# Kernel optimization log

Hardware: AMD Instinct MI355X
Metric: run time of the kernel (lower is better)

## Reference

```python
import math
import jax, jax.numpy as jnp
import numpy as np

HEADS = 8
DIM = 512
HEAD_SIZE = DIM // HEADS  # 64


def setup_inputs() -> dict:
    key = jax.random.key(0)
    ks = jax.random.split(key, 5)
    b, nh, nw, t, d = 16, 16, 16, 16, DIM
    x = jax.random.normal(ks[0], (b, nh, nw, t, d), dtype=jnp.float32)
    s = 1.0 / math.sqrt(d)
    Wq = jax.random.normal(ks[1], (d, d), dtype=jnp.float32) * s
    Wk = jax.random.normal(ks[2], (d, d), dtype=jnp.float32) * s
    Wv = jax.random.normal(ks[3], (d, d), dtype=jnp.float32) * s
    Wo = jax.random.normal(ks[4], (d, d), dtype=jnp.float32) * s
    z = jnp.zeros((d,), dtype=jnp.float32)
    return {"x": x, "Wq": Wq, "bq": z, "Wk": Wk, "bk": z, "Wv": Wv, "bv": z, "Wo": Wo, "bo": z}


def _split_heads(t):
    # [b, n1, n2, T, D] -> [b, n1, n2, H, T, hs]
    b, n1, n2, T, _ = t.shape
    return t.reshape(b, n1, n2, T, HEADS, HEAD_SIZE).transpose(0, 1, 2, 4, 3, 5)


def reference(x, Wq, bq, Wk, bk, Wv, bv, Wo, bo):
    q = _split_heads(x @ Wq + bq)
    k = _split_heads(x @ Wk + bk)
    v = _split_heads(x @ Wv + bv)
    # windowed attention scores: [b, n1, n2, H, T, T]
    scores = jnp.einsum('bnmhtd,bnmhsd->bnmhts', q, k) / math.sqrt(HEAD_SIZE)
    probs = jax.nn.sigmoid(scores)  # NOTE: elementwise sigmoid, not softmax
    ctx = jnp.einsum('bnmhts,bnmhsd->bnmhtd', probs, v)
    b, n1, n2, H, T, hs = ctx.shape
    ctx = ctx.transpose(0, 1, 2, 4, 3, 5).reshape(b, n1, n2, T, H * hs)
    return ctx @ Wo + bo
```

## Files before the change

### kernel.cpp

```cpp
#include <hip/hip_runtime.h>
#include <hip/hip_bf16.h>

typedef float f32x4 __attribute__((ext_vector_type(4)));
typedef __bf16 bf16x8 __attribute__((ext_vector_type(8)));
typedef unsigned short u16x4 __attribute__((ext_vector_type(4)));
typedef unsigned short u16x8 __attribute__((ext_vector_type(8)));

__device__ __forceinline__ unsigned short f2bf(float f) {
  union { float f; unsigned u; } x; x.f = f;
  unsigned r = x.u + 0x7FFFu + ((x.u >> 16) & 1u);
  return (unsigned short)(r >> 16);
}

__device__ __forceinline__ void gl16(const void* g, void* l) {
  __builtin_amdgcn_global_load_lds(
      (const __attribute__((address_space(1))) unsigned*)g,
      (__attribute__((address_space(3))) unsigned*)l, 16, 0, 0);
}

__global__ __launch_bounds__(256) void prep_wt(const float* __restrict__ Wq,
                                               const float* __restrict__ Wk,
                                               const float* __restrict__ Wv,
                                               const float* __restrict__ Wo,
                                               unsigned short* __restrict__ WT) {
  __shared__ unsigned short ts[64][65];
  const float* W = (blockIdx.z == 0) ? Wq : (blockIdx.z == 1) ? Wk
                   : (blockIdx.z == 2) ? Wv : Wo;
  const int t = threadIdx.x;
  const int kbase = blockIdx.y * 64;
  const int nbase = blockIdx.x * 64;
  for (int i = 0; i < 16; ++i) {
    int idx = i * 256 + t;
    int r = idx >> 6, c = idx & 63;
    ts[r][c] = f2bf(W[(size_t)(kbase + r) * 512 + nbase + c]);
  }
  __syncthreads();
  unsigned short* dst = WT + (size_t)blockIdx.z * 512 * 512;
  for (int i = 0; i < 16; ++i) {
    int idx = i * 256 + t;
    int nn = idx >> 6, kk = idx & 63;
    dst[(size_t)(nbase + nn) * 512 + kbase + kk] = ts[kk][nn];
  }
}

__global__ void prep_bias(const float* __restrict__ bq, const float* __restrict__ bk,
                          const float* __restrict__ bv, float* __restrict__ biasc) {
  int i = blockIdx.x * 256 + threadIdx.x;
  if (i < 512) biasc[i] = bq[i];
  else if (i < 1024) biasc[i] = bk[i - 512];
  else if (i < 1536) biasc[i] = bv[i - 1024];
}

__global__ __launch_bounds__(256) void convert_x(const float* __restrict__ x,
                                                 unsigned short* __restrict__ xb,
                                                 long long n8) {
  long long i = (long long)blockIdx.x * 256 + threadIdx.x;
  const long long stride = (long long)gridDim.x * 256;
  for (; i < n8; i += stride) {
    f32x4 a = *reinterpret_cast<const f32x4*>(&x[i * 8]);
    f32x4 b = *reinterpret_cast<const f32x4*>(&x[i * 8 + 4]);
    u16x8 o;
    o[0] = f2bf(a[0]); o[1] = f2bf(a[1]); o[2] = f2bf(a[2]); o[3] = f2bf(a[3]);
    o[4] = f2bf(b[0]); o[5] = f2bf(b[1]); o[6] = f2bf(b[2]); o[7] = f2bf(b[3]);
    *reinterpret_cast<u16x8*>(&xb[i * 8]) = o;
  }
}

template <typename CT>
__global__ __launch_bounds__(512, 2) void gemm256(
    const unsigned short* __restrict__ A, int lda,
    const unsigned short* __restrict__ BT,
    CT* __restrict__ C, int ldc,
    const float* __restrict__ bias, int NB) {
  __shared__ alignas(16) unsigned short pool[66048];
  const int t = threadIdx.x;
  const int lane = t & 63;
  const int w = t >> 6;
  const int wm = w >> 2, wn = w & 3;

  const int nwg = gridDim.x;
  const int cpx = nwg >> 3;
  const int wg = (blockIdx.x & 7) * cpx + (blockIdx.x >> 3);
  const int n0 = (wg % NB) * 256;
  const int m0 = (wg / NB) * 256;

  const int sr = lane >> 3;
  const int sg = ((lane & 7) ^ sr) << 3;
  const unsigned short* gA = A + (size_t)(m0 + w * 8 + sr) * lda + sg;
  const unsigned short* gB = BT + (size_t)(n0 + w * 8 + sr) * 512 + sg;
  const int lw = w * 512;

#define STAGE_A(kt, h, b)                                                   \
  { const unsigned short* g_ = gA + (size_t)(h) * 128 * lda + (kt) * 64;    \
    unsigned short* l_ = &pool[(b) * 16384 + (h) * 8192 + lw];              \
    gl16(g_, l_); gl16(g_ + (size_t)64 * lda, l_ + 4096); }
#define STAGE_B(kt, h, b)                                                   \
  { const unsigned short* g_ = gB + (size_t)(h) * 128 * 512 + (kt) * 64;    \
    unsigned short* l_ = &pool[32768 + (b) * 16384 + (h) * 8192 + lw];      \
    gl16(g_, l_); gl16(g_ + (size_t)64 * 512, l_ + 4096); }

  const int fr = lane & 15;
  const int fg = lane >> 4;
  const int fx = lane & 7;
  auto readA = [&](int b, int mi, int kf) -> bf16x8 {
    return *reinterpret_cast<const bf16x8*>(
        &pool[(b) * 16384 + (wm * 128 + mi * 16 + fr) * 64 +
              ((((kf << 2) + fg) ^ fx) << 3)]);
  };
  auto readB = [&](int b, int ni, int kf) -> bf16x8 {
    return *reinterpret_cast<const bf16x8*>(
        &pool[32768 + (b) * 16384 + (wn * 64 + ni * 16 + fr) * 64 +
              ((((kf << 2) + fg) ^ fx) << 3)]);
  };

  f32x4 acc[8][4];
#pragma unroll
  for (int i = 0; i < 8; ++i)
#pragma unroll
    for (int j = 0; j < 4; ++j) acc[i][j] = (f32x4){0.f, 0.f, 0.f, 0.f};
  bf16x8 bfr[4][2];

#define PHASE(b, q, READB, STAGES, VM)                                       \
  {                                                                          \
    bf16x8 a0_ = readA(b, 2 * (q), 0), a1_ = readA(b, 2 * (q), 1);           \
    bf16x8 a2_ = readA(b, 2 * (q) + 1, 0), a3_ = readA(b, 2 * (q) + 1, 1);   \
    if (READB) {                                                             \
      _Pragma("unroll") for (int ni = 0; ni < 4; ++ni) {                     \
        bfr[ni][0] = readB(b, ni, 0);                                        \
        bfr[ni][1] = readB(b, ni, 1);                                        \
      }                                                                      \
    }                                                                        \
    STAGES;                                                                  \
    if ((VM) == 4) asm volatile("s_waitcnt vmcnt(4)" ::: "memory");          \
    if ((VM) == 0) asm volatile("s_waitcnt vmcnt(0)" ::: "memory");          \
    __builtin_amdgcn_s_barrier();                                            \
    asm volatile("s_waitcnt lgkmcnt(0)" ::: "memory");                       \
    __builtin_amdgcn_sched_barrier(0);                                       \
    __builtin_amdgcn_s_setprio(1);                                           \
    _Pragma("unroll") for (int ni = 0; ni < 4; ++ni) {                       \
      acc[2 * (q)][ni] = __builtin_amdgcn_mfma_f32_16x16x32_bf16(            \
          a0_, bfr[ni][0], acc[2 * (q)][ni], 0, 0, 0);                       \
      acc[2 * (q) + 1][ni] = __builtin_amdgcn_mfma_f32_16x16x32_bf16(        \
          a2_, bfr[ni][0], acc[2 * (q) + 1][ni], 0, 0, 0);                   \
    }                                                                        \
    _Pragma("unroll") for (int ni = 0; ni < 4; ++ni) {                       \
      acc[2 * (q)][ni] = __builtin_amdgcn_mfma_f32_16x16x32_bf16(            \
          a1_, bfr[ni][1], acc[2 * (q)][ni], 0, 0, 0);                       \
      acc[2 * (q) + 1][ni] = __builtin_amdgcn_mfma_f32_16x16x32_bf16(        \
          a3_, bfr[ni][1], acc[2 * (q) + 1][ni], 0, 0, 0);                   \
    }                                                                        \
    __builtin_amdgcn_s_setprio(0);                                           \
    __builtin_amdgcn_s_barrier();                                            \
  }

  STAGE_B(0, 0, 0); STAGE_B(0, 1, 0);
  STAGE_A(0, 0, 0); STAGE_A(0, 1, 0);
  STAGE_B(1, 0, 1); STAGE_B(1, 1, 1);
  asm volatile("s_waitcnt vmcnt(4)" ::: "memory");
  __builtin_amdgcn_s_barrier();

#pragma unroll
  for (int i = 0; i < 4; ++i) {
    const bool s2 = (i < 3);
    const int vmA = s2 ? 4 : 0;
    const int vmB = s2 ? 4 : 0;
    PHASE(0, 0, true,  { STAGE_A(2 * i + 1, 0, 1) }, -1);
    PHASE(0, 1, false, { STAGE_A(2 * i + 1, 1, 1) if (s2) STAGE_B(2 * i + 2, 0, 0) }, -1);
    PHASE(0, 2, false, { if (s2) STAGE_B(2 * i + 2, 1, 0) }, -1);
    PHASE(0, 3, false, {}, vmA);
    PHASE(1, 0, true,  { if (s2) STAGE_A(2 * i + 2, 0, 0) }, -1);
    PHASE(1, 1, false, { if (s2) STAGE_A(2 * i + 2, 1, 0) }, -1);
    PHASE(1, 2, false, { if (s2) STAGE_B(2 * i + 3, 0, 1) }, -1);
    PHASE(1, 3, false, { if (s2) STAGE_B(2 * i + 3, 1, 1) }, vmB);
  }
#undef PHASE
#undef STAGE_A
#undef STAGE_B

  __syncthreads();
  if constexpr (sizeof(CT) == 2) {
#pragma unroll
    for (int ni = 0; ni < 4; ++ni) {
      int cl = wn * 64 + ni * 16 + fr;
      float bc = bias[n0 + cl];
#pragma unroll
      for (int mi = 0; mi < 8; ++mi) {
        int rl = wm * 128 + mi * 16 + fg * 4;
#pragma unroll
        for (int r = 0; r < 4; ++r)
          pool[(rl + r) * 258 + cl] = f2bf(acc[mi][ni][r] + bc);
      }
    }
    __syncthreads();
#pragma unroll
    for (int it = 0; it < 16; ++it) {
      int idx = it * 512 + t;
      int row = idx >> 5, c8 = idx & 31;
      u16x8 v = *reinterpret_cast<const u16x8*>(&pool[row * 258 + c8 * 8]);
      *reinterpret_cast<u16x8*>(&C[(size_t)(m0 + row) * ldc + n0 + c8 * 8]) = v;
    }
  } else {
    float* stf = reinterpret_cast<float*>(pool);
#pragma unroll
    for (int h = 0; h < 2; ++h) {
      if (wm == h) {
#pragma unroll
        for (int ni = 0; ni < 4; ++ni) {
          int cl = wn * 64 + ni * 16 + fr;
          float bc = bias[n0 + cl];
#pragma unroll
          for (int mi = 0; mi < 8; ++mi) {
            int rl = mi * 16 + fg * 4;
#pragma unroll
            for (int r = 0; r < 4; ++r)
              stf[(rl + r) * 258 + cl] = acc[mi][ni][r] + bc;
          }
        }
      }
      __syncthreads();
#pragma unroll
      for (int it = 0; it < 16; ++it) {
        int idx = it * 512 + t;
        int row = idx >> 6, c4 = idx & 63;
        f32x4 v = *reinterpret_cast<const f32x4*>(&stf[row * 258 + c4 * 4]);
        *reinterpret_cast<f32x4*>(
            &C[(size_t)(m0 + h * 128 + row) * ldc + n0 + c4 * 4]) = v;
      }
      __syncthreads();
    }
  }
}

__global__ __launch_bounds__(256) void attn2(unsigned short* __restrict__ QKV) {
  __shared__ alignas(16) unsigned short sh[33792];
  const int VS = 16384, PS = 32768;
  const int t = threadIdx.x;
  const int lane = t & 63;
  const int w = t >> 6;
  const int fr = lane & 15, fg = lane >> 4, fx = lane & 7;
  const int sr = lane >> 3;
  const int sgx = ((lane & 7) ^ sr) << 3;
  const int sgl = (lane & 7) << 3;
  const size_t m0r = (size_t)blockIdx.x * 128;

#define SK2(h, b)                                                            \
  _Pragma("unroll") for (int u = 0; u < 4; ++u) {                            \
    const int r0 = u * 32 + w * 8;                                           \
    gl16(QKV + (m0r + r0 + sr) * 1536 + 512 + (h) * 64 + sgx,                \
         &sh[(b) * 8192 + r0 * 64]);                                         \
  }
#define SV2(h, b)                                                            \
  _Pragma("unroll") for (int u = 0; u < 4; ++u) {                            \
    const int r0 = u * 32 + w * 8;                                           \
    gl16(QKV + (m0r + r0 + sr) * 1536 + 1024 + (h) * 64 + sgl,               \
         &sh[VS + (b) * 8192 + r0 * 64]);                                    \
  }

  SK2(0, 0) SV2(0, 0)
  asm volatile("s_waitcnt vmcnt(0)" ::: "memory");
  __syncthreads();

  for (int h = 0; h < 8; ++h) {
    const int b = h & 1;
    u16x8 q[2][2];
#pragma unroll
    for (int ww = 0; ww < 2; ++ww) {
      const int wi = w * 2 + ww;
      const unsigned short* qrow = QKV + (m0r + wi * 16 + fr) * 1536 + h * 64;
      q[ww][0] = *reinterpret_cast<const u16x8*>(qrow + fg * 8);
      q[ww][1] = *reinterpret_cast<const u16x8*>(qrow + 32 + fg * 8);
    }
    if (h < 7) { SK2(h + 1, b ^ 1) SV2(h + 1, b ^ 1) }

#pragma unroll
    for (int ww = 0; ww < 2; ++ww) {
      const int wi = w * 2 + ww;
      f32x4 s = (f32x4){0.f, 0.f, 0.f, 0.f};
      {
        bf16x8 kf_ = *reinterpret_cast<const bf16x8*>(
            &sh[b * 8192 + (wi * 16 + fr) * 64 + ((fg ^ fx) << 3)]);
        s = __builtin_amdgcn_mfma_f32_16x16x32_bf16(
            kf_, __builtin_bit_cast(bf16x8, q[ww][0]), s, 0, 0, 0);
        kf_ = *reinterpret_cast<const bf16x8*>(
            &sh[b * 8192 + (wi * 16 + fr) * 64 + (((4 + fg) ^ fx) << 3)]);
        s = __builtin_amdgcn_mfma_f32_16x16x32_bf16(
            kf_, __builtin_bit_cast(bf16x8, q[ww][1]), s, 0, 0, 0);
      }
      u16x4 pfu;
#pragma unroll
      for (int r = 0; r < 4; ++r)
        pfu[r] = f2bf(1.0f / (1.0f + __expf(-s[r] * 0.125f)));
      *reinterpret_cast<u16x4*>(&sh[PS + w * 256 + fr * 16 + fg * 4]) = pfu;
      u16x8 pbu = (u16x8){0, 0, 0, 0, 0, 0, 0, 0};
      if (fg < 2)
        pbu = *reinterpret_cast<const u16x8*>(&sh[PS + w * 256 + fr * 16 + fg * 8]);
      bf16x8 pb = __builtin_bit_cast(bf16x8, pbu);
#pragma unroll
      for (int dc = 0; dc < 4; ++dc) {
        u16x8 vau;
#pragma unroll
        for (int j = 0; j < 8; ++j)
          vau[j] = sh[VS + b * 8192 + (wi * 16 + (fg & 1) * 8 + j) * 64 + dc * 16 + fr];
        f32x4 c = __builtin_amdgcn_mfma_f32_16x16x32_bf16(
            __builtin_bit_cast(bf16x8, vau), pb, (f32x4){0.f, 0.f, 0.f, 0.f},
            0, 0, 0);
        u16x4 o;
#pragma unroll
        for (int r = 0; r < 4; ++r) o[r] = f2bf(c[r]);
        *reinterpret_cast<u16x4*>(
            &QKV[(m0r + wi * 16 + fr) * 1536 + 1024 + h * 64 + dc * 16 + fg * 4]) = o;
      }
    }
    asm volatile("s_waitcnt vmcnt(8)" ::: "memory");
    __syncthreads();
  }
#undef SK2
#undef SV2
}

extern "C" void kernel_launch(void* const* d_in, const int* in_sizes, int n_in,
                              void* d_out, int out_size, void* d_ws, size_t ws_size,
                              hipStream_t stream) {
  const float* x  = (const float*)d_in[0];
  const float* Wq = (const float*)d_in[1];
  const float* bq = (const float*)d_in[2];
  const float* Wk = (const float*)d_in[3];
  const float* bk = (const float*)d_in[4];
  const float* Wv = (const float*)d_in[5];
  const float* bv = (const float*)d_in[6];
  const float* Wo = (const float*)d_in[7];
  const float* bo = (const float*)d_in[8];
  float* out = (float*)d_out;

  const int M = 65536;
  char* ws = (char*)d_ws;
  unsigned short* WT = (unsigned short*)ws;
  float* biasc = (float*)(ws + (size_t)2048 * 512 * 2);
  const long long prep_bytes = (long long)2048 * 512 * 2 + 8192;

  prep_wt<<<dim3(8, 8, 4), 256, 0, stream>>>(Wq, Wk, Wv, Wo, WT);
  prep_bias<<<6, 256, 0, stream>>>(bq, bk, bv, biasc);

  long long avail = (long long)ws_size - prep_bytes;
  int chunk_rows = 65536;
  while (chunk_rows > 2048 && (long long)chunk_rows * 4096 > avail) chunk_rows >>= 1;
  const int nchunks = M / chunk_rows;

  unsigned short* Xb  = (unsigned short*)(ws + prep_bytes);
  unsigned short* QKV = Xb + (size_t)chunk_rows * 512;

  for (int c = 0; c < nchunks; ++c) {
    const size_t row0 = (size_t)c * chunk_rows;
    const int mt = chunk_rows / 256;
    convert_x<<<2048, 256, 0, stream>>>(x + row0 * 512, Xb,
                                        (long long)chunk_rows * 64);
    gemm256<unsigned short><<<mt * 6, 512, 0, stream>>>(
        Xb, 512, WT, QKV, 1536, biasc, 6);
    attn2<<<chunk_rows / 128, 256, 0, stream>>>(QKV);
    gemm256<float><<<mt * 2, 512, 0, stream>>>(
        QKV + 1024, 1536, WT + (size_t)1536 * 512, out + row0 * 512, 512, bo, 2);
  }
}
```

Measured before the change: 293.8 us.

## Fuse fp32-to-bf16 conversion of x into the QKV projection GEMM

Removes the separate convert_x kernel and adds a QKV GEMM variant that loads fp32 activations straight into registers, converts them to bf16 and writes them into swizzled LDS, interleaved with the MFMA phases. This drops the bf16 copy of x (a write plus a re-read of 64 MB of bf16) and shrinks the workspace needed per chunk. In exchange the GEMM reads fp32 A, twice the bytes per tile, and each of the 6 N-tiles per row block re-reads it. The A path also uses register staging instead of direct global-to-LDS loads, which adds VGPR pressure and conversion ALU work inside the pipelined loop.

```diff
diff --git a/kernel.cpp b/kernel.cpp
--- a/kernel.cpp
+++ b/kernel.cpp
@@ -51,18 +51,154 @@
   else if (i < 1536) biasc[i] = bv[i - 1024];
 }
 
-__global__ __launch_bounds__(256) void convert_x(const float* __restrict__ x,
-                                                 unsigned short* __restrict__ xb,
-                                                 long long n8) {
-  long long i = (long long)blockIdx.x * 256 + threadIdx.x;
-  const long long stride = (long long)gridDim.x * 256;
-  for (; i < n8; i += stride) {
-    f32x4 a = *reinterpret_cast<const f32x4*>(&x[i * 8]);
-    f32x4 b = *reinterpret_cast<const f32x4*>(&x[i * 8 + 4]);
-    u16x8 o;
-    o[0] = f2bf(a[0]); o[1] = f2bf(a[1]); o[2] = f2bf(a[2]); o[3] = f2bf(a[3]);
-    o[4] = f2bf(b[0]); o[5] = f2bf(b[1]); o[6] = f2bf(b[2]); o[7] = f2bf(b[3]);
-    *reinterpret_cast<u16x8*>(&xb[i * 8]) = o;
+__global__ __launch_bounds__(512, 2) void gemm256_f32a(
+    const float* __restrict__ A, int lda,
+    const unsigned short* __restrict__ BT,
+    unsigned short* __restrict__ C, int ldc,
+    const float* __restrict__ bias, int NB) {
+  __shared__ alignas(16) unsigned short pool[66048];
+  const int t = threadIdx.x;
+  const int lane = t & 63;
+  const int w = t >> 6;
+  const int wm = w >> 2, wn = w & 3;
+
+  const int nwg = gridDim.x;
+  const int cpx = nwg >> 3;
+  const int wg = (blockIdx.x & 7) * cpx + (blockIdx.x >> 3);
+  const int n0 = (wg % NB) * 256;
+  const int m0 = (wg / NB) * 256;
+
+  const int sr = lane >> 3;
+  const int sg = ((lane & 7) ^ sr) << 3;
+  const unsigned short* gB = BT + (size_t)(n0 + w * 8 + sr) * 512 + sg;
+  const int lw = w * 512;
+#define SBa(kt, b)                                                          \
+  { const unsigned short* g_ = gB + (kt) * 64;                              \
+    unsigned short* l_ = &pool[32768 + (b) * 16384 + lw];                   \
+    gl16(g_, l_); gl16(g_ + (size_t)64 * 512, l_ + 4096); }
+#define SBb(kt, b)                                                          \
+  { const unsigned short* g_ = gB + (size_t)128 * 512 + (kt) * 64;          \
+    unsigned short* l_ = &pool[32768 + (b) * 16384 + 8192 + lw];            \
+    gl16(g_, l_); gl16(g_ + (size_t)64 * 512, l_ + 4096); }
+
+  const int arow = t >> 3;
+  const int aseg = t & 7;
+  const float* gA = A + (size_t)(m0 + arow) * lda + ((aseg ^ (arow & 7)) << 3);
+  f32x4 ar0[8], ar1[8];
+#define LA(u, arr, kt)                                                      \
+  { const float* g_ = gA + (size_t)(u) * 64 * lda + (kt) * 64;              \
+    arr[2 * (u)] = *reinterpret_cast<const f32x4*>(g_);                     \
+    arr[2 * (u) + 1] = *reinterpret_cast<const f32x4*>(g_ + 4); }
+#define WAu(u, arr, b)                                                      \
+  { bf16x8 pk_;                                                             \
+    _Pragma("unroll") for (int j_ = 0; j_ < 4; ++j_) {                      \
+      pk_[j_] = (__bf16)arr[2 * (u)][j_];                                   \
+      pk_[4 + j_] = (__bf16)arr[2 * (u) + 1][j_];                           \
+    }                                                                       \
+    *reinterpret_cast<bf16x8*>(                                             \
+        &pool[(b) * 16384 + (arow + (u) * 64) * 64 + (aseg << 3)]) = pk_; }
+
+  const int fr = lane & 15;
+  const int fg = lane >> 4;
+  const int fx = lane & 7;
+  auto readA = [&](int b, int mi, int kf) -> bf16x8 {
+    return *reinterpret_cast<const bf16x8*>(
+        &pool[(b) * 16384 + (wm * 128 + mi * 16 + fr) * 64 +
+              ((((kf << 2) + fg) ^ fx) << 3)]);
+  };
+  auto readB = [&](int b, int ni, int kf) -> bf16x8 {
+    return *reinterpret_cast<const bf16x8*>(
+        &pool[32768 + (b) * 16384 + (wn * 64 + ni * 16 + fr) * 64 +
+              ((((kf << 2) + fg) ^ fx) << 3)]);
+  };
+
+  f32x4 acc[8][4];
+#pragma unroll
+  for (int i = 0; i < 8; ++i)
+#pragma unroll
+    for (int j = 0; j < 4; ++j) acc[i][j] = (f32x4){0.f, 0.f, 0.f, 0.f};
+  bf16x8 bfr[4][2];
+
+#define PHASEF(b, q, READB, STAGES, VM)                                      \
+  {                                                                          \
+    bf16x8 a0_ = readA(b, 2 * (q), 0), a1_ = readA(b, 2 * (q), 1);           \
+    bf16x8 a2_ = readA(b, 2 * (q) + 1, 0), a3_ = readA(b, 2 * (q) + 1, 1);   \
+    if (READB) {                                                             \
+      _Pragma("unroll") for (int ni = 0; ni < 4; ++ni) {                     \
+        bfr[ni][0] = readB(b, ni, 0);                                        \
+        bfr[ni][1] = readB(b, ni, 1);                                        \
+      }                                                                      \
+    }                                                                        \
+    STAGES;                                                                  \
+    if ((VM) == 12)                                                          \
+      asm volatile("s_waitcnt vmcnt(12) lgkmcnt(0)" ::: "memory");           \
+    if ((VM) == 0)                                                           \
+      asm volatile("s_waitcnt vmcnt(0) lgkmcnt(0)" ::: "memory");            \
+    __builtin_amdgcn_s_barrier();                                            \
+    asm volatile("s_waitcnt lgkmcnt(0)" ::: "memory");                       \
+    __builtin_amdgcn_sched_barrier(0);                                       \
+    __builtin_amdgcn_s_setprio(1);                                           \
+    _Pragma("unroll") for (int ni = 0; ni < 4; ++ni) {                       \
+      acc[2 * (q)][ni] = __builtin_amdgcn_mfma_f32_16x16x32_bf16(            \
+          a0_, bfr[ni][0], acc[2 * (q)][ni], 0, 0, 0);                       \
+      acc[2 * (q) + 1][ni] = __builtin_amdgcn_mfma_f32_16x16x32_bf16(        \
+          a2_, bfr[ni][0], acc[2 * (q) + 1][ni], 0, 0, 0);                   \
+    }                                                                        \
+    _Pragma("unroll") for (int ni = 0; ni < 4; ++ni) {                       \
+      acc[2 * (q)][ni] = __builtin_amdgcn_mfma_f32_16x16x32_bf16(            \
+          a1_, bfr[ni][1], acc[2 * (q)][ni], 0, 0, 0);                       \
+      acc[2 * (q) + 1][ni] = __builtin_amdgcn_mfma_f32_16x16x32_bf16(        \
+          a3_, bfr[ni][1], acc[2 * (q) + 1][ni], 0, 0, 0);                   \
+    }                                                                        \
+    __builtin_amdgcn_s_setprio(0);                                           \
+    __builtin_amdgcn_s_barrier();                                            \
+  }
+
+  LA(0, ar0, 0) LA(1, ar0, 0) LA(2, ar0, 0) LA(3, ar0, 0)
+  LA(0, ar1, 1) LA(1, ar1, 1) LA(2, ar1, 1) LA(3, ar1, 1)
+  SBa(0, 0) SBb(0, 0) SBa(1, 1) SBb(1, 1)
+  WAu(0, ar0, 0) WAu(1, ar0, 0) WAu(2, ar0, 0) WAu(3, ar0, 0)
+  asm volatile("s_waitcnt vmcnt(4) lgkmcnt(0)" ::: "memory");
+  __builtin_amdgcn_s_barrier();
+
+#pragma unroll
+  for (int i = 0; i < 4; ++i) {
+    const bool s2 = (i < 3);
+    PHASEF(0, 0, true,  { if (s2) { LA(0, ar0, 2 * i + 2) LA(1, ar0, 2 * i + 2) } }, -1);
+    PHASEF(0, 1, false, { if (s2) { LA(2, ar0, 2 * i + 2) LA(3, ar0, 2 * i + 2) SBa(2 * i + 2, 0) } }, -1);
+    PHASEF(0, 2, false, { WAu(0, ar1, 1) WAu(1, ar1, 1) if (s2) SBb(2 * i + 2, 0) }, -1);
+    PHASEF(0, 3, false, { WAu(2, ar1, 1) WAu(3, ar1, 1) }, s2 ? 12 : 0);
+    PHASEF(1, 0, true,  { if (s2) { LA(0, ar1, 2 * i + 3) LA(1, ar1, 2 * i + 3) } }, -1);
+    PHASEF(1, 1, false, { if (s2) { LA(2, ar1, 2 * i + 3) LA(3, ar1, 2 * i + 3) } }, -1);
+    PHASEF(1, 2, false, { if (s2) { SBa(2 * i + 3, 1) WAu(0, ar0, 0) WAu(1, ar0, 0) } }, -1);
+    PHASEF(1, 3, false, { if (s2) { SBb(2 * i + 3, 1) WAu(2, ar0, 0) WAu(3, ar0, 0) } }, s2 ? 12 : -1);
+  }
+#undef PHASEF
+#undef SBa
+#undef SBb
+#undef LA
+#undef WAu
+
+  __syncthreads();
+#pragma unroll
+  for (int ni = 0; ni < 4; ++ni) {
+    int cl = wn * 64 + ni * 16 + fr;
+    float bc = bias[n0 + cl];
+#pragma unroll
+    for (int mi = 0; mi < 8; ++mi) {
+      int rl = wm * 128 + mi * 16 + fg * 4;
+#pragma unroll
+      for (int r = 0; r < 4; ++r)
+        pool[(rl + r) * 258 + cl] = f2bf(acc[mi][ni][r] + bc);
+    }
+  }
+  __syncthreads();
+#pragma unroll
+  for (int it = 0; it < 16; ++it) {
+    int idx = it * 512 + t;
+    int row = idx >> 5, c8 = idx & 31;
+    u16x8 v = *reinterpret_cast<const u16x8*>(&pool[row * 258 + c8 * 8]);
+    *reinterpret_cast<u16x8*>(&C[(size_t)(m0 + row) * ldc + n0 + c8 * 8]) = v;
   }
 }
 
@@ -343,19 +479,16 @@
 
   long long avail = (long long)ws_size - prep_bytes;
   int chunk_rows = 65536;
-  while (chunk_rows > 2048 && (long long)chunk_rows * 4096 > avail) chunk_rows >>= 1;
+  while (chunk_rows > 2048 && (long long)chunk_rows * 3072 > avail) chunk_rows >>= 1;
   const int nchunks = M / chunk_rows;
 
-  unsigned short* Xb  = (unsigned short*)(ws + prep_bytes);
-  unsigned short* QKV = Xb + (size_t)chunk_rows * 512;
+  unsigned short* QKV = (unsigned short*)(ws + prep_bytes);
 
   for (int c = 0; c < nchunks; ++c) {
     const size_t row0 = (size_t)c * chunk_rows;
     const int mt = chunk_rows / 256;
-    convert_x<<<2048, 256, 0, stream>>>(x + row0 * 512, Xb,
-                                        (long long)chunk_rows * 64);
-    gemm256<unsigned short><<<mt * 6, 512, 0, stream>>>(
-        Xb, 512, WT, QKV, 1536, biasc, 6);
+    gemm256_f32a<<<mt * 6, 512, 0, stream>>>(
+        x + row0 * 512, 512, WT, QKV, 1536, biasc, 6);
     attn2<<<chunk_rows / 128, 256, 0, stream>>>(QKV);
     gemm256<float><<<mt * 2, 512, 0, stream>>>(
         QKV + 1024, 1536, WT + (size_t)1536 * 512, out + row0 * 512, 512, bo, 2);
```

New measurement: 420.4 us. 1.43x slower.
